# Kernel optimization log

Hardware: AMD Instinct MI355X
Metric: run time of the kernel (lower is better)

The kernel has to match this reference:

```python
import jax, jax.numpy as jnp
import numpy as np

B, S, DIM, H = 2, 2048, 2048, 16
NOPE, ROPE, VHD, KLR = 128, 64, 128, 512
QKHD = NOPE + ROPE  # 192
SCALE = QKHD ** -0.5
EPS = 1.1920929e-07  # torch.finfo(float32).eps, nn.RMSNorm default eps


def _rope(x, cos, sin):
    # x: [b, s, h, r]; cos/sin: [s, r//2]; pairs are adjacent elements (view_as_complex convention)
    x2 = x.reshape(*x.shape[:-1], -1, 2)
    xr, xi = x2[..., 0], x2[..., 1]
    c = cos[None, :, None, :]
    s_ = sin[None, :, None, :]
    out = jnp.stack([xr * c - xi * s_, xr * s_ + xi * c], axis=-1)
    return out.reshape(x.shape)


def setup_inputs() -> dict:
    key = jax.random.key(0)
    ks = jax.random.split(key, 5)
    x = jax.random.normal(ks[0], (B, S, DIM), jnp.float32)
    wq = jax.random.normal(ks[1], (H * QKHD, DIM), jnp.float32) * 0.02
    wkv_a = jax.random.normal(ks[2], (KLR + ROPE, DIM), jnp.float32) * 0.02
    kv_norm_w = jnp.ones((KLR,), jnp.float32)
    wkv_b = jax.random.normal(ks[3], (H * (NOPE + VHD), KLR), jnp.float32) * 0.02
    wo = jax.random.normal(ks[4], (DIM, H * VHD), jnp.float32) * 0.02
    # rotary tables (start_pos=0, no YaRN since rope_factor=1 / original_seq_len=None)
    inv_freq = 1.0 / (10000.0 ** (np.arange(0, ROPE, 2, dtype=np.float32) / ROPE))
    ang = np.outer(np.arange(S, dtype=np.float32), inv_freq)
    freqs_cos = jnp.asarray(np.cos(ang))
    freqs_sin = jnp.asarray(np.sin(ang))
    # causal mask [S, S]
    mask = jnp.where(jnp.tril(jnp.ones((S, S), bool)), 0.0, -1e9).astype(jnp.float32)
    return {"x": x, "wq": wq, "wkv_a": wkv_a, "kv_norm_w": kv_norm_w,
            "wkv_b": wkv_b, "wo": wo, "freqs_cos": freqs_cos,
            "freqs_sin": freqs_sin, "mask": mask}


def reference(x, wq, wkv_a, kv_norm_w, wkv_b, wo, freqs_cos, freqs_sin, mask):
    b, s, _ = x.shape
    # query projection (q_lora_rank == 0 path)
    q = (x @ wq.T).reshape(b, s, H, QKHD)
    q_nope, q_pe = q[..., :NOPE], q[..., NOPE:]
    q_pe = _rope(q_pe, freqs_cos, freqs_sin)
    # latent KV projection
    kv = x @ wkv_a.T  # [b, s, KLR + ROPE]
    kv_c, k_pe = kv[..., :KLR], kv[..., KLR:]
    kv_c = kv_c * jax.lax.rsqrt(jnp.mean(kv_c * kv_c, axis=-1, keepdims=True) + EPS) * kv_norm_w
    k_pe = _rope(k_pe[:, :, None, :], freqs_cos, freqs_sin)[:, :, 0]  # [b, s, ROPE]
    # KV-absorption: fold wkv_b's K half into the query
    wb = wkv_b.reshape(H, NOPE + VHD, KLR)
    q_proj = jnp.einsum('bshd,hdc->bshc', q_nope, wb[:, :NOPE])  # [b,s,H,KLR]
    scores = (jnp.einsum('bshc,btc->bsht', q_proj, kv_c)
              + jnp.einsum('bshr,btr->bsht', q_pe, k_pe)) * SCALE
    scores = scores + mask[:, None, :]  # broadcast over heads
    attn = jax.nn.softmax(scores.astype(jnp.float32), axis=-1).astype(x.dtype)
    o = jnp.einsum('bsht,btc->bshc', attn, kv_c)
    o = jnp.einsum('bshc,hdc->bshd', o, wb[:, NOPE:])  # value up-projection
    return o.reshape(b, s, H * VHD) @ wo.T
```

## Files before the change

### kernel.cpp

```cpp
#include <hip/hip_runtime.h>

#define DI __device__ __forceinline__

typedef __bf16 bf16x8 __attribute__((ext_vector_type(8)));
typedef float  f32x4  __attribute__((ext_vector_type(4)));

DI unsigned short f2bf(float f){
  unsigned u = __builtin_bit_cast(unsigned, f);
  u = (u + 0x7fffu + ((u >> 16) & 1u)) >> 16;
  return (unsigned short)u;
}
DI float b2f(unsigned short h){
  return __builtin_bit_cast(float, (unsigned)h << 16);
}
DI f32x4 MFMA(bf16x8 a, bf16x8 b, f32x4 c){
  return __builtin_amdgcn_mfma_f32_16x16x32_bf16(a, b, c, 0, 0, 0);
}
DI void gll16(const void* g, void* l){
  __builtin_amdgcn_global_load_lds((const __attribute__((address_space(1))) void*)g,
                                   (__attribute__((address_space(3))) void*)l,
                                   16, 0, 0);
}


__global__ void k_f2b(const float* __restrict__ in, unsigned short* __restrict__ out, long n){
  long i = ((long)blockIdx.x*256 + threadIdx.x)*4;
  if (i >= n) return;
  float4 v = *(const float4*)(in + i);
  ushort4 r; r.x=f2bf(v.x); r.y=f2bf(v.y); r.z=f2bf(v.z); r.w=f2bf(v.w);
  *(ushort4*)(out + i) = r;
}

__global__ void k_wkva(const float* __restrict__ in, unsigned short* __restrict__ out){
  int idx = blockIdx.x*256 + threadIdx.x;
  long i = (long)idx*4;
  int row = (int)(i >> 11), col = (int)(i & 2047);
  ushort4 r;
  if (row < 576){
    float4 v = *(const float4*)(in + (long)row*2048 + col);
    r.x=f2bf(v.x); r.y=f2bf(v.y); r.z=f2bf(v.z); r.w=f2bf(v.w);
  } else { r.x=0; r.y=0; r.z=0; r.w=0; }
  *(ushort4*)(out + i) = r;
}

__global__ void k_wbkT(const float* __restrict__ wkvb, unsigned short* __restrict__ out){
  int i = blockIdx.x*256 + threadIdx.x;
  int d = i & 127, c = (i>>7)&511, h = i>>16;
  out[i] = f2bf(wkvb[(long)((h<<8) + d)*512 + c]);
}

__global__ void k_ropeq(const unsigned short* __restrict__ q, const float* __restrict__ fc,
                        const float* __restrict__ fs, unsigned short* __restrict__ qkcat){
  int i = blockIdx.x*256 + threadIdx.x;
  int p = i & 31, h = (i>>5)&15, m = i>>9;
  int s = m & 2047;
  const unsigned short* qp = q + (long)m*3072 + h*192 + 128 + (p<<1);
  float xr = b2f(qp[0]), xi = b2f(qp[1]);
  float c = fc[(s<<5)+p], sn = fs[(s<<5)+p];
  unsigned short* dst = qkcat + ((long)m*16 + h)*576 + 512 + (p<<1);
  dst[0] = f2bf(xr*c - xi*sn);
  dst[1] = f2bf(xr*sn + xi*c);
}

__global__ void k_ropek(const unsigned short* __restrict__ kv, const float* __restrict__ fc,
                        const float* __restrict__ fs, unsigned short* __restrict__ kvcat){
  int i = blockIdx.x*256 + threadIdx.x;
  int p = i & 31, m = i>>5;
  int s = m & 2047;
  const unsigned short* kp = kv + (long)m*640 + 512 + (p<<1);
  float xr = b2f(kp[0]), xi = b2f(kp[1]);
  float c = fc[(s<<5)+p], sn = fs[(s<<5)+p];
  unsigned short* dst = kvcat + (long)m*576 + 512 + (p<<1);
  dst[0] = f2bf(xr*c - xi*sn);
  dst[1] = f2bf(xr*sn + xi*c);
}

__global__ __launch_bounds__(256)
void k_kvnorm(const unsigned short* __restrict__ kv, const float* __restrict__ w,
              unsigned short* __restrict__ kvcat){
  int m = blockIdx.x*4 + (threadIdx.x>>6);
  int l = threadIdx.x & 63;
  const unsigned short* row = kv + (long)m*640 + (l<<3);
  float v[8]; float ss = 0.f;
  #pragma unroll
  for (int j=0;j<8;j++){ v[j] = b2f(row[j]); ss += v[j]*v[j]; }
  #pragma unroll
  for (int d=1; d<64; d<<=1) ss += __shfl_xor(ss, d, 64);
  float r = rsqrtf(ss*(1.f/512.f) + 1.1920929e-07f);
  unsigned short* dst = kvcat + (long)m*576 + (l<<3);
  const float* wp = w + (l<<3);
  #pragma unroll
  for (int j=0;j<8;j++) dst[j] = f2bf(v[j]*r*wp[j]);
}

__global__ void k_vt(const unsigned short* __restrict__ kvcat, unsigned short* __restrict__ vt){
  int i = blockIdx.x*256 + threadIdx.x;
  int t = i & 2047, c = (i>>11)&511, b = i>>20;
  vt[i] = kvcat[(long)((b<<11)+t)*576 + c];
}

template<int BF16OUT>
__global__ __launch_bounds__(256, 2)
void gemm_bt(const unsigned short* __restrict__ A, const unsigned short* __restrict__ B,
             void* __restrict__ Cv, int K, int lda, int ldb, int ldc,
             long bsA, long bsB, long bsC)
{
  const int bz = blockIdx.z;
  A += (long)bz*bsA; B += (long)bz*bsB;
  const int m0 = blockIdx.x<<7, n0 = blockIdx.y<<7;
  __shared__ __align__(16) unsigned short lA[128*32];
  __shared__ __align__(16) unsigned short lB[128*32];
  const int tid = threadIdx.x, l = tid&63, w = tid>>6;
  const int li = l&15, g = l>>4;
  const int wm = (w>>1)<<6, wn = (w&1)<<6;
  const int r0 = (l>>2), ce = (l&3)<<3;
  f32x4 acc[4][4];
  #pragma unroll
  for (int a_=0;a_<4;a_++)
    #pragma unroll
    for (int b_=0;b_<4;b_++) acc[a_][b_] = f32x4{0.f,0.f,0.f,0.f};

  for (int k0 = 0; k0 < K; k0 += 32){
    __syncthreads();
    #pragma unroll
    for (int i=0;i<2;i++){
      const int ch = (i<<2) + w;
      const int r  = (ch<<4) + r0;
      gll16(A + (long)(m0+r)*lda + k0 + ce, (char*)lA + (ch<<10));
      gll16(B + (long)(n0+r)*ldb + k0 + ce, (char*)lB + (ch<<10));
    }
    __syncthreads();
    bf16x8 af[4], bfv[4];
    #pragma unroll
    for (int mf=0;mf<4;mf++)
      af[mf] = *(const bf16x8*)((const char*)lA + (wm + (mf<<4) + li)*64 + (g<<4));
    #pragma unroll
    for (int nf=0;nf<4;nf++)
      bfv[nf] = *(const bf16x8*)((const char*)lB + (wn + (nf<<4) + li)*64 + (g<<4));
    #pragma unroll
    for (int mf=0;mf<4;mf++)
      #pragma unroll
      for (int nf=0;nf<4;nf++)
        acc[mf][nf] = MFMA(af[mf], bfv[nf], acc[mf][nf]);
  }
  #pragma unroll
  for (int mf=0;mf<4;mf++)
    #pragma unroll
    for (int nf=0;nf<4;nf++)
      #pragma unroll
      for (int j=0;j<4;j++){
        const int row = m0 + wm + (mf<<4) + (g<<2) + j;
        const int col = n0 + wn + (nf<<4) + li;
        if (BF16OUT)
          ((unsigned short*)Cv)[(long)bz*bsC + (long)row*ldc + col] = f2bf(acc[mf][nf][j]);
        else
          ((float*)Cv)[(long)bz*bsC + (long)row*ldc + col] = acc[mf][nf][j];
      }
}

#define SCALE_F 0.07216878364870322f

__global__ __launch_bounds__(512, 2)
void attn(const unsigned short* __restrict__ qk,
          const unsigned short* __restrict__ kvc,
          const unsigned short* __restrict__ vt,
          unsigned short* __restrict__ o)
{
  const int pi = blockIdx.x, hp = blockIdx.y, b = blockIdx.z;
  const int tid = threadIdx.x, l = tid & 63, w = tid >> 6;
  const int li = l & 15, g = l >> 4;
  const int h  = (hp << 1) + (w >> 2);
  const int rg = w & 3;

  __shared__ __align__(16) unsigned short Kl[2][32*576];
  __shared__ __align__(16) unsigned short Vl[2][512*32];
  __shared__ __align__(16) unsigned short Pl[8][16*40];
  unsigned short* Pw = &Pl[w][0];

  int soff[9];
  const unsigned short* sbase;
  if (w < 4){
    sbase = kvc + (long)(b << 11) * 576;
    #pragma unroll
    for (int i = 0; i < 9; i++){
      int ch = i*256 + tid;
      int r  = ch / 72;
      int cb = (ch - r*72) << 4;
      int cbs = cb ^ ((r & 7) << 4);
      soff[i] = r*576 + (cbs >> 1);
    }
  } else {
    sbase = vt + (long)(b << 9) * 2048;
    #pragma unroll
    for (int i = 0; i < 8; i++){
      int ch = i*256 + (tid - 256);
      int c  = ch >> 2;
      int tb = (ch & 3) << 4;
      int tbs = tb ^ ((c & 3) << 4);
      soff[i] = c*2048 + (tbs >> 1);
    }
    soff[8] = 0;
  }

  auto STAGE = [&](int buf, int kt){
    const int t0 = kt << 5;
    if (w < 4){
      const unsigned short* s = sbase + (long)t0 * 576;
      char* d = (char*)&Kl[buf][0] + tid*16;
      #pragma unroll
      for (int i = 0; i < 9; i++) gll16(s + soff[i], d + i*4096);
    } else {
      const unsigned short* s = sbase + t0;
      char* d = (char*)&Vl[buf][0] + (tid - 256)*16;
      #pragma unroll
      for (int i = 0; i < 8; i++) gll16(s + soff[i], d + i*4096);
    }
  };

  #pragma unroll 1
  for (int half = 0; half < 2; half++){
    const int qt = half ? (31 - pi) : pi;
    const int q0 = (qt << 6) + (rg << 4);
    const int nsteps = (qt << 1) + 2;

    bf16x8 qf[18];
    {
      const unsigned short* qp = qk + ((long)((b<<11) + q0 + li)*16 + h)*576 + (g<<3);
      #pragma unroll
      for (int ks = 0; ks < 18; ks++) qf[ks] = *(const bf16x8*)(qp + ks*32);
    }
    asm volatile("s_waitcnt vmcnt(0)" ::: "memory");
    __builtin_amdgcn_sched_barrier(0);

    f32x4 accO[32];
    #pragma unroll
    for (int i = 0; i < 32; i++) accO[i] = f32x4{0.f,0.f,0.f,0.f};
    float mrow[4] = {-1e30f,-1e30f,-1e30f,-1e30f};
    float lrow[4] = {0.f,0.f,0.f,0.f};

    STAGE(0, 0);
    int cur = 0;

    #pragma unroll 1
    for (int kt = 0; kt < nsteps; kt++){
      const int tn = (kt + 1 < nsteps) ? kt + 1 : kt;
      STAGE(cur ^ 1, tn);
      if (w < 4) asm volatile("s_waitcnt vmcnt(9)" ::: "memory");
      else       asm volatile("s_waitcnt vmcnt(8)" ::: "memory");
      __builtin_amdgcn_sched_barrier(0);
      __builtin_amdgcn_s_barrier();

      const int t0 = kt << 5;
      const char* Kb = (const char*)&Kl[cur][0];
      const char* Vb = (const char*)&Vl[cur][0];
      f32x4 sc0 = f32x4{0.f,0.f,0.f,0.f}, sc1 = f32x4{0.f,0.f,0.f,0.f};
      const int swz = (li & 7) << 4;
      #pragma unroll
      for (int ks = 0; ks < 18; ks++){
        const int cb = ((ks<<6) + (g<<4)) ^ swz;
        bf16x8 k0 = *(const bf16x8*)(Kb + li*1152 + cb);
        bf16x8 k1 = *(const bf16x8*)(Kb + (16+li)*1152 + cb);
        sc0 = MFMA(qf[ks], k0, sc0);
        sc1 = MFMA(qf[ks], k1, sc1);
      }
      float corr[4];
      #pragma unroll
      for (int j = 0; j < 4; j++){
        const int q = q0 + (g<<2) + j;
        float s0 = sc0[j]*SCALE_F;
        float s1 = sc1[j]*SCALE_F;
        if (t0 + li      > q) s0 = -1e30f;
        if (t0 + 16 + li > q) s1 = -1e30f;
        float mx = fmaxf(s0, s1);
        #pragma unroll
        for (int d = 1; d < 16; d <<= 1) mx = fmaxf(mx, __shfl_xor(mx, d, 64));
        const float mnew = fmaxf(mrow[j], mx);
        corr[j] = __expf(mrow[j] - mnew);
        mrow[j] = mnew;
        const float p0 = __expf(s0 - mnew);
        const float p1 = __expf(s1 - mnew);
        float rs = p0 + p1;
        #pragma unroll
        for (int d = 1; d < 16; d <<= 1) rs += __shfl_xor(rs, d, 64);
        lrow[j] = lrow[j]*corr[j] + rs;
        Pw[((g<<2)+j)*40 + li]      = f2bf(p0);
        Pw[((g<<2)+j)*40 + 16 + li] = f2bf(p1);
      }
      #pragma unroll
      for (int nf = 0; nf < 32; nf++){
        f32x4 a = accO[nf];
        a[0]*=corr[0]; a[1]*=corr[1]; a[2]*=corr[2]; a[3]*=corr[3];
        accO[nf] = a;
      }
      asm volatile("s_waitcnt lgkmcnt(0)" ::: "memory");
      __builtin_amdgcn_sched_barrier(0);
      const bf16x8 pa = *(const bf16x8*)((const char*)Pw + li*80 + (g<<4));
      #pragma unroll
      for (int nf = 0; nf < 32; nf++){
        const int c = (nf<<4) + li;
        bf16x8 vb = *(const bf16x8*)(Vb + c*64 + ((g<<4) ^ ((c&3)<<4)));
        accO[nf] = MFMA(pa, vb, accO[nf]);
      }
      __builtin_amdgcn_sched_barrier(0);
      __builtin_amdgcn_s_barrier();
      cur ^= 1;
    }

    #pragma unroll
    for (int j = 0; j < 4; j++){
      const float inv = 1.0f/lrow[j];
      const int q = q0 + (g<<2) + j;
      unsigned short* op = o + ((long)((b<<11) + q)*16 + h)*512 + li;
      #pragma unroll
      for (int nf = 0; nf < 32; nf++) op[nf<<4] = f2bf(accO[nf][j]*inv);
    }
  }
}


extern "C" void kernel_launch(void* const* d_in, const int* in_sizes, int n_in,
                              void* d_out, int out_size, void* d_ws, size_t ws_size,
                              hipStream_t stream)
{
  const float* x    = (const float*)d_in[0];
  const float* wq   = (const float*)d_in[1];
  const float* wkva = (const float*)d_in[2];
  const float* kvw  = (const float*)d_in[3];
  const float* wkvb = (const float*)d_in[4];
  const float* wo   = (const float*)d_in[5];
  const float* fc   = (const float*)d_in[6];
  const float* fs   = (const float*)d_in[7];
  float* out = (float*)d_out;

  char* ws = (char*)d_ws;
  auto alloc = [&](size_t bytes)->void*{
    void* p = ws; ws += (bytes + 255) & ~(size_t)255; return p;
  };
  unsigned short* x_bf    = (unsigned short*)alloc( 8388608ull*2);
  unsigned short* wq_bf   = (unsigned short*)alloc( 6291456ull*2);
  unsigned short* wkva_p  = (unsigned short*)alloc( 1310720ull*2);
  unsigned short* wkvb_bf = (unsigned short*)alloc( 2097152ull*2);
  unsigned short* wbkT    = (unsigned short*)alloc( 1048576ull*2);
  unsigned short* wo_bf   = (unsigned short*)alloc( 4194304ull*2);
  unsigned short* q_bf    = (unsigned short*)alloc(12582912ull*2);
  unsigned short* kv_bf   = (unsigned short*)alloc( 2621440ull*2);
  unsigned short* qkcat   = (unsigned short*)alloc(37748736ull*2);
  unsigned short* kvcat   = (unsigned short*)alloc( 2359296ull*2);
  unsigned short* vtb     = (unsigned short*)alloc( 2097152ull*2);
  unsigned short* obuf    = (unsigned short*)alloc(33554432ull*2);
  unsigned short* o2      = (unsigned short*)alloc( 8388608ull*2);

  k_f2b <<<8192,256,0,stream>>>(x,    x_bf,    8388608);
  k_f2b <<<6144,256,0,stream>>>(wq,   wq_bf,   6291456);
  k_wkva<<<1280,256,0,stream>>>(wkva, wkva_p);
  k_f2b <<<2048,256,0,stream>>>(wkvb, wkvb_bf, 2097152);
  k_wbkT<<<4096,256,0,stream>>>(wkvb, wbkT);
  k_f2b <<<4096,256,0,stream>>>(wo,   wo_bf,   4194304);

  gemm_bt<1><<<dim3(32,24,1),256,0,stream>>>(x_bf, wq_bf, q_bf, 2048, 2048, 2048, 3072, 0,0,0);
  gemm_bt<1><<<dim3(32,5,1),256,0,stream>>>(x_bf, wkva_p, kv_bf, 2048, 2048, 2048, 640, 0,0,0);

  k_ropeq <<<8192,256,0,stream>>>(q_bf, fc, fs, qkcat);
  k_kvnorm<<<1024,256,0,stream>>>(kv_bf, kvw, kvcat);
  k_ropek <<<512, 256,0,stream>>>(kv_bf, fc, fs, kvcat);

  gemm_bt<1><<<dim3(32,4,16),256,0,stream>>>(q_bf, wbkT, qkcat, 128, 3072, 128, 9216,
                                             192, 65536, 576);
  k_vt<<<8192,256,0,stream>>>(kvcat, vtb);

  attn<<<dim3(16,8,2),512,0,stream>>>(qkcat, kvcat, vtb, obuf);

  gemm_bt<1><<<dim3(32,1,16),256,0,stream>>>(obuf, wkvb_bf + 65536, o2, 512, 8192, 512, 2048,
                                             512, 131072, 128);
  gemm_bt<0><<<dim3(32,16,1),256,0,stream>>>(o2, wo_bf, out, 2048, 2048, 2048, 2048, 0,0,0);
}
```

Measured before the change: 799.8 us.

## Drop LDS staging of V, read it from global and widen the K tile to 64

The attention kernel now stages only the latent K tile into LDS, doubled from 32 to 64 keys per step, with all 512 threads issuing the async loads. The transposed V operand is read straight from global memory in the PV matmul, split into two 32-key halves that reuse the per-wave P scratch buffer. The aim is to halve the number of loop iterations and barriers and to free LDS that was spent on V. The cost is PV operand loads that now go through global memory and cache instead of LDS, which can stall the MFMAs.

```diff
diff --git a/kernel.cpp b/kernel.cpp
--- a/kernel.cpp
+++ b/kernel.cpp
@@ -172,56 +172,34 @@
   const int h  = (hp << 1) + (w >> 2);
   const int rg = w & 3;
 
-  __shared__ __align__(16) unsigned short Kl[2][32*576];
-  __shared__ __align__(16) unsigned short Vl[2][512*32];
+  __shared__ __align__(16) unsigned short Kl[2][64*576];
   __shared__ __align__(16) unsigned short Pl[8][16*40];
   unsigned short* Pw = &Pl[w][0];
 
   int soff[9];
-  const unsigned short* sbase;
-  if (w < 4){
-    sbase = kvc + (long)(b << 11) * 576;
-    #pragma unroll
-    for (int i = 0; i < 9; i++){
-      int ch = i*256 + tid;
-      int r  = ch / 72;
-      int cb = (ch - r*72) << 4;
-      int cbs = cb ^ ((r & 7) << 4);
-      soff[i] = r*576 + (cbs >> 1);
-    }
-  } else {
-    sbase = vt + (long)(b << 9) * 2048;
-    #pragma unroll
-    for (int i = 0; i < 8; i++){
-      int ch = i*256 + (tid - 256);
-      int c  = ch >> 2;
-      int tb = (ch & 3) << 4;
-      int tbs = tb ^ ((c & 3) << 4);
-      soff[i] = c*2048 + (tbs >> 1);
-    }
-    soff[8] = 0;
+  #pragma unroll
+  for (int i = 0; i < 9; i++){
+    int ch = i*512 + tid;
+    int r  = ch / 72;
+    int c  = ch - r*72;
+    int cs = c ^ (r & 7);
+    soff[i] = r*576 + (cs << 3);
   }
+  const unsigned short* sbase = kvc + (long)(b << 11)*576;
+  const unsigned short* vbase = vt  + (long)(b << 9)*2048;
 
   auto STAGE = [&](int buf, int kt){
-    const int t0 = kt << 5;
-    if (w < 4){
-      const unsigned short* s = sbase + (long)t0 * 576;
-      char* d = (char*)&Kl[buf][0] + tid*16;
-      #pragma unroll
-      for (int i = 0; i < 9; i++) gll16(s + soff[i], d + i*4096);
-    } else {
-      const unsigned short* s = sbase + t0;
-      char* d = (char*)&Vl[buf][0] + (tid - 256)*16;
-      #pragma unroll
-      for (int i = 0; i < 8; i++) gll16(s + soff[i], d + i*4096);
-    }
+    const unsigned short* s = sbase + (long)(kt << 6)*576;
+    char* d = (char*)&Kl[buf][0] + tid*16;
+    #pragma unroll
+    for (int i = 0; i < 9; i++) gll16(s + soff[i], d + i*8192);
   };
 
   #pragma unroll 1
   for (int half = 0; half < 2; half++){
     const int qt = half ? (31 - pi) : pi;
     const int q0 = (qt << 6) + (rg << 4);
-    const int nsteps = (qt << 1) + 2;
+    const int nsteps = qt + 1;
 
     bf16x8 qf[18];
     {
@@ -245,46 +223,53 @@
     for (int kt = 0; kt < nsteps; kt++){
       const int tn = (kt + 1 < nsteps) ? kt + 1 : kt;
       STAGE(cur ^ 1, tn);
-      if (w < 4) asm volatile("s_waitcnt vmcnt(9)" ::: "memory");
-      else       asm volatile("s_waitcnt vmcnt(8)" ::: "memory");
+      asm volatile("s_waitcnt vmcnt(9)" ::: "memory");
       __builtin_amdgcn_sched_barrier(0);
       __builtin_amdgcn_s_barrier();
 
-      const int t0 = kt << 5;
+      const int t0 = kt << 6;
       const char* Kb = (const char*)&Kl[cur][0];
-      const char* Vb = (const char*)&Vl[cur][0];
-      f32x4 sc0 = f32x4{0.f,0.f,0.f,0.f}, sc1 = f32x4{0.f,0.f,0.f,0.f};
-      const int swz = (li & 7) << 4;
+
+      f32x4 sc[4];
+      sc[0] = f32x4{0.f,0.f,0.f,0.f}; sc[1] = sc[0]; sc[2] = sc[0]; sc[3] = sc[0];
       #pragma unroll
       for (int ks = 0; ks < 18; ks++){
-        const int cb = ((ks<<6) + (g<<4)) ^ swz;
-        bf16x8 k0 = *(const bf16x8*)(Kb + li*1152 + cb);
-        bf16x8 k1 = *(const bf16x8*)(Kb + (16+li)*1152 + cb);
-        sc0 = MFMA(qf[ks], k0, sc0);
-        sc1 = MFMA(qf[ks], k1, sc1);
-      }
+        const int cb = (ks<<6) + (g<<4);
+        #pragma unroll
+        for (int n = 0; n < 4; n++){
+          const int tt = (n<<4) + li;
+          bf16x8 kf = *(const bf16x8*)(Kb + tt*1152 + (cb ^ ((tt&7)<<4)));
+          sc[n] = MFMA(qf[ks], kf, sc[n]);
+        }
+      }
+
       float corr[4];
+      unsigned pp[2][4];
       #pragma unroll
       for (int j = 0; j < 4; j++){
         const int q = q0 + (g<<2) + j;
-        float s0 = sc0[j]*SCALE_F;
-        float s1 = sc1[j]*SCALE_F;
-        if (t0 + li      > q) s0 = -1e30f;
-        if (t0 + 16 + li > q) s1 = -1e30f;
-        float mx = fmaxf(s0, s1);
+        float s_[4];
+        #pragma unroll
+        for (int n = 0; n < 4; n++){
+          s_[n] = sc[n][j]*SCALE_F;
+          if (t0 + (n<<4) + li > q) s_[n] = -1e30f;
+        }
+        float mx = fmaxf(fmaxf(s_[0], s_[1]), fmaxf(s_[2], s_[3]));
         #pragma unroll
         for (int d = 1; d < 16; d <<= 1) mx = fmaxf(mx, __shfl_xor(mx, d, 64));
         const float mnew = fmaxf(mrow[j], mx);
         corr[j] = __expf(mrow[j] - mnew);
         mrow[j] = mnew;
-        const float p0 = __expf(s0 - mnew);
-        const float p1 = __expf(s1 - mnew);
-        float rs = p0 + p1;
+        float p0 = __expf(s_[0] - mnew);
+        float p1 = __expf(s_[1] - mnew);
+        float p2 = __expf(s_[2] - mnew);
+        float p3 = __expf(s_[3] - mnew);
+        float rs = (p0 + p1) + (p2 + p3);
         #pragma unroll
         for (int d = 1; d < 16; d <<= 1) rs += __shfl_xor(rs, d, 64);
         lrow[j] = lrow[j]*corr[j] + rs;
-        Pw[((g<<2)+j)*40 + li]      = f2bf(p0);
-        Pw[((g<<2)+j)*40 + 16 + li] = f2bf(p1);
+        pp[0][j] = (unsigned)f2bf(p0) | ((unsigned)f2bf(p1) << 16);
+        pp[1][j] = (unsigned)f2bf(p2) | ((unsigned)f2bf(p3) << 16);
       }
       #pragma unroll
       for (int nf = 0; nf < 32; nf++){
@@ -292,14 +277,28 @@
         a[0]*=corr[0]; a[1]*=corr[1]; a[2]*=corr[2]; a[3]*=corr[3];
         accO[nf] = a;
       }
-      asm volatile("s_waitcnt lgkmcnt(0)" ::: "memory");
-      __builtin_amdgcn_sched_barrier(0);
-      const bf16x8 pa = *(const bf16x8*)((const char*)Pw + li*80 + (g<<4));
-      #pragma unroll
-      for (int nf = 0; nf < 32; nf++){
-        const int c = (nf<<4) + li;
-        bf16x8 vb = *(const bf16x8*)(Vb + c*64 + ((g<<4) ^ ((c&3)<<4)));
-        accO[nf] = MFMA(pa, vb, accO[nf]);
+
+      #pragma unroll
+      for (int kh = 0; kh < 2; kh++){
+        #pragma unroll
+        for (int j = 0; j < 4; j++){
+          Pw[((g<<2)+j)*40 + li]      = (unsigned short)(pp[kh][j] & 0xffffu);
+          Pw[((g<<2)+j)*40 + 16 + li] = (unsigned short)(pp[kh][j] >> 16);
+        }
+        asm volatile("s_waitcnt lgkmcnt(0)" ::: "memory");
+        __builtin_amdgcn_sched_barrier(0);
+        const bf16x8 pa = *(const bf16x8*)((const char*)Pw + li*80 + (g<<4));
+        const unsigned short* vrow = vbase + t0 + (kh<<5) + (g<<3);
+        #pragma unroll 4
+        for (int nf = 0; nf < 32; nf++){
+          const int c = (nf<<4) + li;
+          bf16x8 vb = *(const bf16x8*)(vrow + (long)c*2048);
+          accO[nf] = MFMA(pa, vb, accO[nf]);
+        }
+        if (kh == 0){
+          asm volatile("s_waitcnt lgkmcnt(0)" ::: "memory");
+          __builtin_amdgcn_sched_barrier(0);
+        }
       }
       __builtin_amdgcn_sched_barrier(0);
       __builtin_amdgcn_s_barrier();
```

Result: slower. 2.619 ms (+227.4%).

## Use lazy softmax rescaling with deferred row-sum reduction and MFMA priority hints

Applied to the files above, without the earlier changes.

The online softmax now rescales the running max and the accumulators only when some wave lane sees a score more than 8 above the current max (a warp-wide any-vote). Otherwise it reuses the stale max, which skips the max shuffles and the rescale of 128 accumulator values in most iterations. Per-lane partial row sums are accumulated and reduced with shuffles only once in the epilogue, and s_setprio hints are placed around the MFMA loops. This adds a divergent branch and lets exp values reach up to e^8 before rescaling, which stays inside fp32 and bf16 range but slightly changes rounding.

```diff
diff --git a/kernel.cpp b/kernel.cpp
--- a/kernel.cpp
+++ b/kernel.cpp
@@ -236,7 +236,7 @@
     #pragma unroll
     for (int i = 0; i < 32; i++) accO[i] = f32x4{0.f,0.f,0.f,0.f};
     float mrow[4] = {-1e30f,-1e30f,-1e30f,-1e30f};
-    float lrow[4] = {0.f,0.f,0.f,0.f};
+    float lsum[4] = {0.f,0.f,0.f,0.f};
 
     STAGE(0, 0);
     int cur = 0;
@@ -255,6 +255,7 @@
       const char* Vb = (const char*)&Vl[cur][0];
       f32x4 sc0 = f32x4{0.f,0.f,0.f,0.f}, sc1 = f32x4{0.f,0.f,0.f,0.f};
       const int swz = (li & 7) << 4;
+      __builtin_amdgcn_s_setprio(1);
       #pragma unroll
       for (int ks = 0; ks < 18; ks++){
         const int cb = ((ks<<6) + (g<<4)) ^ swz;
@@ -263,44 +264,59 @@
         sc0 = MFMA(qf[ks], k0, sc0);
         sc1 = MFMA(qf[ks], k1, sc1);
       }
-      float corr[4];
+      __builtin_amdgcn_s_setprio(0);
+
+      float s0v[4], s1v[4];
       #pragma unroll
       for (int j = 0; j < 4; j++){
         const int q = q0 + (g<<2) + j;
-        float s0 = sc0[j]*SCALE_F;
-        float s1 = sc1[j]*SCALE_F;
-        if (t0 + li      > q) s0 = -1e30f;
-        if (t0 + 16 + li > q) s1 = -1e30f;
-        float mx = fmaxf(s0, s1);
+        s0v[j] = sc0[j]*SCALE_F;
+        s1v[j] = sc1[j]*SCALE_F;
+        if (t0 + li      > q) s0v[j] = -1e30f;
+        if (t0 + 16 + li > q) s1v[j] = -1e30f;
+      }
+      bool viol = false;
+      #pragma unroll
+      for (int j = 0; j < 4; j++)
+        viol = viol || (fmaxf(s0v[j], s1v[j]) > mrow[j] + 8.0f);
+      if (__any(viol)){
+        float cr[4];
         #pragma unroll
-        for (int d = 1; d < 16; d <<= 1) mx = fmaxf(mx, __shfl_xor(mx, d, 64));
-        const float mnew = fmaxf(mrow[j], mx);
-        corr[j] = __expf(mrow[j] - mnew);
-        mrow[j] = mnew;
-        const float p0 = __expf(s0 - mnew);
-        const float p1 = __expf(s1 - mnew);
-        float rs = p0 + p1;
+        for (int j = 0; j < 4; j++){
+          float mx = fmaxf(s0v[j], s1v[j]);
+          #pragma unroll
+          for (int d = 1; d < 16; d <<= 1) mx = fmaxf(mx, __shfl_xor(mx, d, 64));
+          const float mnew = fmaxf(mrow[j], mx);
+          cr[j] = __expf(mrow[j] - mnew);
+          mrow[j] = mnew;
+          lsum[j] *= cr[j];
+        }
         #pragma unroll
-        for (int d = 1; d < 16; d <<= 1) rs += __shfl_xor(rs, d, 64);
-        lrow[j] = lrow[j]*corr[j] + rs;
+        for (int nf = 0; nf < 32; nf++){
+          f32x4 a = accO[nf];
+          a[0]*=cr[0]; a[1]*=cr[1]; a[2]*=cr[2]; a[3]*=cr[3];
+          accO[nf] = a;
+        }
+      }
+      #pragma unroll
+      for (int j = 0; j < 4; j++){
+        const float p0 = __expf(s0v[j] - mrow[j]);
+        const float p1 = __expf(s1v[j] - mrow[j]);
+        lsum[j] += p0 + p1;
         Pw[((g<<2)+j)*40 + li]      = f2bf(p0);
         Pw[((g<<2)+j)*40 + 16 + li] = f2bf(p1);
-      }
-      #pragma unroll
-      for (int nf = 0; nf < 32; nf++){
-        f32x4 a = accO[nf];
-        a[0]*=corr[0]; a[1]*=corr[1]; a[2]*=corr[2]; a[3]*=corr[3];
-        accO[nf] = a;
       }
       asm volatile("s_waitcnt lgkmcnt(0)" ::: "memory");
       __builtin_amdgcn_sched_barrier(0);
       const bf16x8 pa = *(const bf16x8*)((const char*)Pw + li*80 + (g<<4));
+      __builtin_amdgcn_s_setprio(1);
       #pragma unroll
       for (int nf = 0; nf < 32; nf++){
         const int c = (nf<<4) + li;
         bf16x8 vb = *(const bf16x8*)(Vb + c*64 + ((g<<4) ^ ((c&3)<<4)));
         accO[nf] = MFMA(pa, vb, accO[nf]);
       }
+      __builtin_amdgcn_s_setprio(0);
       __builtin_amdgcn_sched_barrier(0);
       __builtin_amdgcn_s_barrier();
       cur ^= 1;
@@ -308,7 +324,10 @@
 
     #pragma unroll
     for (int j = 0; j < 4; j++){
-      const float inv = 1.0f/lrow[j];
+      float ls = lsum[j];
+      #pragma unroll
+      for (int d = 1; d < 16; d <<= 1) ls += __shfl_xor(ls, d, 64);
+      const float inv = 1.0f/ls;
       const int q = q0 + (g<<2) + j;
       unsigned short* op = o + ((long)((b<<11) + q)*16 + h)*512 + li;
       #pragma unroll
```

Result: faster. 698.3 us (-12.7%).
